# Optimization experiments

Hardware: AMD Instinct MI355X
Metric: run time of the kernel (lower is better)

The kernel has to match this reference:

```python
import jax, jax.numpy as jnp
import numpy as np

SIGMA = 25.0
EPS = 1e-5
TWO_PI = 2.0 * np.pi


def _gn(x, gamma, beta, groups):
    # GroupNorm over (C//G, H, W) per group, per-channel affine.
    B, C, H, W = x.shape
    xg = x.reshape(B, groups, -1)
    m = xg.mean(-1, keepdims=True)
    v = xg.var(-1, keepdims=True)
    xn = ((xg - m) * jax.lax.rsqrt(v + EPS)).reshape(B, C, H, W)
    return xn * gamma[None, :, None, None] + beta[None, :, None, None]


def _conv3(x, k, b):
    y = jax.lax.conv_general_dilated(x, k, (1, 1), 'SAME',
                                     dimension_numbers=('NCHW', 'OIHW', 'NCHW'))
    return y + b[None, :, None, None]


def _tconv2(x, k, b):
    # ConvTranspose2d kernel=2 stride=2 (no overlap) == einsum + reshape.
    # k: [C_in, C_out, 2, 2]
    B, C, H, W = x.shape
    O = k.shape[1]
    y = jnp.einsum('bchw,codq->bohdwq', x, k).reshape(B, O, 2 * H, 2 * W)
    return y + b[None, :, None, None]


def _conv1(x, k, b):
    # 1x1 conv; k: [C_out, C_in]
    return jnp.einsum('bchw,oc->bohw', x, k) + b[None, :, None, None]


def _pool(x):
    B, C, H, W = x.shape
    return x.reshape(B, C, H // 2, 2, W // 2, 2).max(axis=(3, 5))


def _std(t):
    return jnp.sqrt((SIGMA ** (2.0 * t) - 1.0) / (2.0 * jnp.log(SIGMA)))


def setup_inputs() -> dict:
    key = jax.random.key(0)
    ks = jax.random.split(key, 16)
    B, H, W = 64, 128, 128
    E = 2 * W  # 256 = embed_dim

    def w(k, shape, fan_in):
        return jax.random.normal(k, shape, jnp.float32) / np.sqrt(fan_in)

    inp = {
        'x': jax.random.normal(ks[0], (B, 1, H, W), jnp.float32),
        't': jax.random.uniform(ks[1], (B,), jnp.float32, 1e-3, 1.0),
        'Wf': jax.random.normal(ks[2], (H, W), jnp.float32) * 30.0,  # fixed Fourier features
        'fc1_w': w(ks[3], (E, E), E),
        'fc1_b': jnp.zeros((E,), jnp.float32),
        'conv1_k': w(ks[4], (6, 1, 3, 3), 9),
        'conv1_b': jnp.zeros((6,), jnp.float32),
        'gn1_g': jnp.ones((6,), jnp.float32), 'gn1_b': jnp.zeros((6,), jnp.float32),
        'conv2_k': w(ks[5], (24, 6, 3, 3), 6 * 9),
        'conv2_b': jnp.zeros((24,), jnp.float32),
        'gn2_g': jnp.ones((24,), jnp.float32), 'gn2_b': jnp.zeros((24,), jnp.float32),
        't3_k': w(ks[6], (24, 24, 2, 2), 24 * 4),
        't3_b': jnp.zeros((24,), jnp.float32),
        'gn3_g': jnp.ones((48,), jnp.float32), 'gn3_b': jnp.zeros((48,), jnp.float32),
        't4_k': w(ks[7], (48, 12, 2, 2), 48 * 4),
        't4_b': jnp.zeros((12,), jnp.float32),
        'gn4_g': jnp.ones((18,), jnp.float32), 'gn4_b': jnp.zeros((18,), jnp.float32),
        't5_k': w(ks[8], (6, 18), 18),
        't5_b': jnp.zeros((6,), jnp.float32),
        'gn5_g': jnp.ones((6,), jnp.float32), 'gn5_b': jnp.zeros((6,), jnp.float32),
        'fin_k': w(ks[9], (1, 6), 6),
        'fin_b': jnp.zeros((1,), jnp.float32),
    }
    return inp


def reference(x, t, Wf, fc1_w, fc1_b, conv1_k, conv1_b, gn1_g, gn1_b,
              conv2_k, conv2_b, gn2_g, gn2_b, t3_k, t3_b, gn3_g, gn3_b,
              t4_k, t4_b, gn4_g, gn4_b, t5_k, t5_b, gn5_g, gn5_b,
              fin_k, fin_b):
    # Vectorized Gaussian Fourier projection: [B,1,H,W] -> [B,1,H,2W]
    p = x * Wf[None, None] * TWO_PI
    xe = jnp.concatenate([jnp.sin(p), jnp.cos(p)], axis=-1)
    # fc1 on last dim (embed_dim = 2W)
    xf = jnp.einsum('bchw,ow->bcho', xe, fc1_w) + fc1_b
    c1 = _conv3(xf, conv1_k, conv1_b)                              # [B,6,H,2W]
    p1 = _pool(jax.nn.relu(_gn(c1, gn1_g, gn1_b, 6)))              # [B,6,H/2,W]
    c2 = _conv3(p1, conv2_k, conv2_b)                              # [B,24,H/2,W]
    p2 = _pool(jax.nn.relu(_gn(c2, gn2_g, gn2_b, 24)))             # [B,24,H/4,W/2]
    a = p2 * jax.nn.sigmoid(p2)                                    # SiLU bottleneck
    u3 = _tconv2(a, t3_k, t3_b)                                    # [B,24,H/2,W]
    g3 = _gn(jnp.concatenate([c2, u3], axis=1), gn3_g, gn3_b, 6)   # 48 ch
    u4 = _tconv2(g3, t4_k, t4_b)                                   # [B,12,H,2W]
    g4 = _gn(jnp.concatenate([c1, u4], axis=1), gn4_g, gn4_b, 6)   # 18 ch
    u5 = _conv1(g4, t5_k, t5_b)                                    # [B,6,H,2W]
    g5 = _gn(u5, gn5_g, gn5_b, 6)
    return _conv1(g5, fin_k, fin_b) / _std(t)[:, None, None, None]
```

## Files before the change

kernel.cpp:

```cpp
#include <hip/hip_runtime.h>
#include <hip/hip_bf16.h>
#include <math.h>

#define BB 64
#define HH 128
#define WW 128
#define EE 256
#define HP (HH*EE)
#define H2 64
#define W2 128
#define PL2 (H2*W2)
#define H4 32
#define W4 64
#define PL4 (H4*W4)

typedef __hip_bfloat16 bf;
typedef unsigned short ushortt;
typedef __attribute__((ext_vector_type(8))) __bf16 b8v;
typedef __attribute__((ext_vector_type(4))) float f4v;

__device__ __forceinline__ float tof(bf v)    { return __bfloat162float(v); }
__device__ __forceinline__ bf    tob(float v) { return __float2bfloat16(v); }
__device__ __forceinline__ unsigned int bfbits(float v) {
    return (unsigned int)__builtin_bit_cast(ushortt, __float2bfloat16(v));
}
__device__ __forceinline__ float b2f(unsigned int u16) {
    unsigned int x = u16 << 16;
    return __builtin_bit_cast(float, x);
}
__device__ __forceinline__ void wred2(float& s, float& q) {
    #pragma unroll
    for (int m = 32; m; m >>= 1) {
        s += __shfl_xor(s, m);
        q += __shfl_xor(q, m);
    }
}

__global__ __launch_bounds__(256) void k_fourier_fc1(
    const float* __restrict__ x, const float* __restrict__ Wf,
    const float* __restrict__ fc1_w, const float* __restrict__ fc1_b,
    bf* __restrict__ xf, float* __restrict__ mb)
{
    __shared__ ushortt sA[64*264];
    __shared__ ushortt sB[64*264];
    int t = threadIdx.x;
    for (int i = blockIdx.x*256 + t; i < 9216; i += 512*256) mb[i] = 0.f;
    int rb = blockIdx.x >> 2, cb = blockIdx.x & 3;
    int row0 = rb*64, col0 = cb*64;
    const float TP = 6.2831853071795864769f;
    for (int it = 0; it < 32; ++it) {
        int i = it*256 + t;
        int r = i >> 7, w = i & 127;
        int rg = row0 + r;
        float p = x[(size_t)rg*WW + w] * Wf[(size_t)(rg & (HH-1))*WW + w] * TP;
        sA[r*264 + w]       = (ushortt)bfbits(__sinf(p));
        sA[r*264 + 128 + w] = (ushortt)bfbits(__cosf(p));
    }
    #pragma unroll
    for (int it = 0; it < 16; ++it) {
        int i = it*256 + t;
        int o = i >> 6, c4 = i & 63;
        float4 w4 = *(const float4*)(fc1_w + (size_t)(col0 + o)*EE + c4*4);
        uint2 pk;
        pk.x = bfbits(w4.x) | (bfbits(w4.y) << 16);
        pk.y = bfbits(w4.z) | (bfbits(w4.w) << 16);
        *(uint2*)&sB[o*264 + c4*4] = pk;
    }
    __syncthreads();
    int lane = t & 63, wid = t >> 6;
    int m = lane & 15, kq = (lane >> 4) * 8;
    f4v acc[4] = {};
    const ushortt* aBase = &sA[(wid*16 + m)*264 + kq];
    #pragma unroll
    for (int k0 = 0; k0 < 8; ++k0) {
        b8v av = *(const b8v*)(aBase + k0*32);
        #pragma unroll
        for (int t4 = 0; t4 < 4; ++t4) {
            b8v bv = *(const b8v*)&sB[(t4*16 + m)*264 + k0*32 + kq];
            acc[t4] = __builtin_amdgcn_mfma_f32_16x16x32_bf16(av, bv, acc[t4], 0, 0, 0);
        }
    }
    int rbase = row0 + wid*16 + (lane >> 4)*4;
    #pragma unroll
    for (int t4 = 0; t4 < 4; ++t4) {
        int col = col0 + t4*16 + m;
        float bias = fc1_b[col];
        #pragma unroll
        for (int r = 0; r < 4; ++r)
            xf[(size_t)(rbase + r)*EE + col] = tob(acc[t4][r] + bias);
    }
}

__global__ __launch_bounds__(256) void k_conv1(
    const bf* __restrict__ xf, const float* __restrict__ k,
    const float* __restrict__ bias, bf* __restrict__ c1, float* __restrict__ mc1)
{
    __shared__ ushortt sT[6*272];
    __shared__ float red[4][6][2];
    int t = threadIdx.x;
    int ht = blockIdx.x & 31, b = blockIdx.x >> 5;
    int h0 = ht*4;
    const bf* src = xf + (size_t)b*HP;
    if (t < 192) {
        int r = t >> 5, i = t & 31;
        int gy = h0 - 1 + r;
        uint4 v = {0,0,0,0};
        if (gy >= 0 && gy < HH) v = *(const uint4*)(src + (size_t)gy*EE + i*8);
        *(uint4*)&sT[r*272 + 8 + i*8] = v;
    } else if (t < 204) {
        int e = t - 192;
        int r = e >> 1, s = e & 1;
        uint4 z = {0,0,0,0};
        *(uint4*)&sT[r*272 + s*264] = z;
    }
    __syncthreads();
    int wq = (t & 63)*4, hl = t >> 6;
    int lane = t & 63, wid = t >> 6;
    float v[3][6];
    #pragma unroll
    for (int ky = 0; ky < 3; ++ky)
      #pragma unroll
      for (int j = 0; j < 6; ++j)
        v[ky][j] = b2f((unsigned)sT[(hl+ky)*272 + 7 + wq + j]);
    int h = h0 + hl;
    #pragma unroll
    for (int o = 0; o < 6; ++o) {
        float bv = bias[o];
        float a0=bv, a1=bv, a2=bv, a3=bv;
        #pragma unroll
        for (int ky = 0; ky < 3; ++ky)
          #pragma unroll
          for (int kx = 0; kx < 3; ++kx) {
            float wv = k[o*9 + ky*3 + kx];
            a0 += v[ky][kx+0]*wv;
            a1 += v[ky][kx+1]*wv;
            a2 += v[ky][kx+2]*wv;
            a3 += v[ky][kx+3]*wv;
          }
        uint2 pk;
        pk.x = bfbits(a0) | (bfbits(a1) << 16);
        pk.y = bfbits(a2) | (bfbits(a3) << 16);
        *(uint2*)(c1 + ((size_t)(b*6+o)*HH + h)*EE + wq) = pk;
        float s = a0+a1+a2+a3, q = a0*a0+a1*a1+a2*a2+a3*a3;
        wred2(s, q);
        if (lane == 0) { red[wid][o][0] = s; red[wid][o][1] = q; }
    }
    __syncthreads();
    if (t < 6) {
        float S = 0.f, Q = 0.f;
        #pragma unroll
        for (int wv = 0; wv < 4; ++wv) { S += red[wv][t][0]; Q += red[wv][t][1]; }
        atomicAdd(&mc1[((size_t)b*6 + t)*2],     S);
        atomicAdd(&mc1[((size_t)b*6 + t)*2 + 1], Q);
    }
}

__global__ __launch_bounds__(256) void k_conv2(
    const bf* __restrict__ c1, const float* __restrict__ mc1,
    const float* __restrict__ g1, const float* __restrict__ be1,
    const float* __restrict__ kw, const float* __restrict__ bias,
    bf* __restrict__ c2, float* __restrict__ mc2)
{
    __shared__ ushortt sA[256*64];
    __shared__ ushortt sW[32*64];
    __shared__ ushortt sP[6*4*136];
    __shared__ float ssl[12];
    __shared__ float redS[24], redQ[24];
    int t = threadIdx.x;
    int ht = blockIdx.x & 31, b = blockIdx.x >> 5;
    int h0 = ht*2;
    int lane = t & 63, wid = t >> 6;
    int m = lane & 15, q4 = lane >> 4;
    if (t < 24) { redS[t] = 0.f; redQ[t] = 0.f; }
    if (t < 6) {
        float s = mc1[((size_t)b*6 + t)*2], q = mc1[((size_t)b*6 + t)*2 + 1];
        float mean = s * (1.f/HP);
        float var  = q * (1.f/HP) - mean*mean;
        float rstd = rsqrtf(var + 1e-5f);
        float sc = g1[t]*rstd;
        ssl[t*2] = sc; ssl[t*2+1] = be1[t] - mean*sc;
    }
    for (int i = t; i < 1024; i += 256) ((unsigned*)sW)[i] = 0;
    __syncthreads();
    for (int i = t; i < 3120; i += 256) {
        int c = i / 520, rem = i % 520;
        int ry = rem / 130, rx = rem % 130;
        int gy = h0 - 1 + ry, gx = rx - 1;
        float v = 0.f;
        if (gy >= 0 && gy < H2 && gx >= 0 && gx < W2) {
            const bf* pp = c1 + ((size_t)(b*6+c)*HH + 2*gy)*EE + 2*gx;
            unsigned r0 = *(const unsigned*)pp;
            unsigned r1 = *(const unsigned*)(pp + EE);
            float sc = ssl[c*2], sh = ssl[c*2+1];
            float e0 = fmaxf(b2f(r0 & 0xffff)*sc+sh, 0.f);
            float e1 = fmaxf(b2f(r0 >> 16)   *sc+sh, 0.f);
            float e2 = fmaxf(b2f(r1 & 0xffff)*sc+sh, 0.f);
            float e3 = fmaxf(b2f(r1 >> 16)   *sc+sh, 0.f);
            v = fmaxf(fmaxf(e0,e1), fmaxf(e2,e3));
        }
        sP[c*544 + ry*136 + rx] = (ushortt)bfbits(v);
    }
    for (int e = t; e < 1296; e += 256) {
        int o = e / 54, kk = e % 54;
        sW[o*64 + ((((kk >> 3) ^ (o & 7)) << 3) | (kk & 7))] = (ushortt)bfbits(kw[e]);
    }
    __syncthreads();
    {
        int r = t >> 7, xx = t & 127;
        unsigned u[32];
        #pragma unroll
        for (int p = 0; p < 27; ++p) {
            int k0 = 2*p, k1 = 2*p + 1;
            int c0 = k0/9, y0 = (k0%9)/3, x0 = k0%3;
            int c1i = k1/9, y1 = (k1%9)/3, x1 = k1%3;
            unsigned lo = sP[c0*544 + (r+y0)*136 + xx + x0];
            unsigned hi = sP[c1i*544 + (r+y1)*136 + xx + x1];
            u[p] = lo | (hi << 16);
        }
        #pragma unroll
        for (int p = 27; p < 32; ++p) u[p] = 0;
        #pragma unroll
        for (int e = 0; e < 8; ++e) {
            uint4 pk; pk.x = u[4*e]; pk.y = u[4*e+1]; pk.z = u[4*e+2]; pk.w = u[4*e+3];
            *(uint4*)&sA[t*64 + ((e ^ (t & 7)) << 3)] = pk;
        }
    }
    __syncthreads();
    b8v wv[2][2];
    #pragma unroll
    for (int nt = 0; nt < 2; ++nt) {
        int o = nt*16 + m;
        #pragma unroll
        for (int ks = 0; ks < 2; ++ks)
            wv[nt][ks] = *(const b8v*)&sW[o*64 + (((ks*4 + q4) ^ (o & 7)) << 3)];
    }
    f4v acc[4][2] = {};
    #pragma unroll
    for (int mt = 0; mt < 4; ++mt) {
        int px = wid*64 + mt*16 + m;
        b8v a0 = *(const b8v*)&sA[px*64 + (((q4)     ^ (px & 7)) << 3)];
        b8v a1 = *(const b8v*)&sA[px*64 + (((4 + q4) ^ (px & 7)) << 3)];
        #pragma unroll
        for (int nt = 0; nt < 2; ++nt) {
            acc[mt][nt] = __builtin_amdgcn_mfma_f32_16x16x32_bf16(a0, wv[nt][0], acc[mt][nt], 0, 0, 0);
            acc[mt][nt] = __builtin_amdgcn_mfma_f32_16x16x32_bf16(a1, wv[nt][1], acc[mt][nt], 0, 0, 0);
        }
    }
    float sAcc[2] = {0.f, 0.f}, qAcc[2] = {0.f, 0.f};
    #pragma unroll
    for (int nt = 0; nt < 2; ++nt) {
        int o = nt*16 + m;
        bool valid = (o < 24);
        float bo = valid ? bias[o] : 0.f;
        #pragma unroll
        for (int mt = 0; mt < 4; ++mt) {
            int pxb = wid*64 + mt*16 + q4*4;
            unsigned l0 = bfbits(acc[mt][nt][0] + bo);
            unsigned l1 = bfbits(acc[mt][nt][1] + bo);
            unsigned l2 = bfbits(acc[mt][nt][2] + bo);
            unsigned l3 = bfbits(acc[mt][nt][3] + bo);
            if (valid) {
                uint2 pk; pk.x = l0 | (l1 << 16); pk.y = l2 | (l3 << 16);
                int r = pxb >> 7, xx = pxb & 127;
                *(uint2*)(c2 + ((size_t)(b*24+o))*PL2 + (size_t)(h0 + r)*W2 + xx) = pk;
                float f0 = b2f(l0), f1 = b2f(l1), f2 = b2f(l2), f3 = b2f(l3);
                sAcc[nt] += f0+f1+f2+f3;
                qAcc[nt] += f0*f0+f1*f1+f2*f2+f3*f3;
            }
        }
    }
    #pragma unroll
    for (int nt = 0; nt < 2; ++nt) {
        int o = nt*16 + m;
        float s = sAcc[nt], q = qAcc[nt];
        s += __shfl_xor(s, 16); q += __shfl_xor(q, 16);
        s += __shfl_xor(s, 32); q += __shfl_xor(q, 32);
        if (q4 == 0 && o < 24) { atomicAdd(&redS[o], s); atomicAdd(&redQ[o], q); }
    }
    __syncthreads();
    if (t < 24) {
        atomicAdd(&mc2[((size_t)b*24 + t)*2],     redS[t]);
        atomicAdd(&mc2[((size_t)b*24 + t)*2 + 1], redQ[t]);
    }
}

__global__ __launch_bounds__(256) void k_tconv3(
    const bf* __restrict__ c2, const float* __restrict__ mc2,
    const float* __restrict__ g2, const float* __restrict__ be2,
    const float* __restrict__ k3, const float* __restrict__ b3,
    bf* __restrict__ u3, float* __restrict__ mu3)
{
    __shared__ ushortt sA[256*64];
    __shared__ ushortt sW[96*64];
    __shared__ float redS[24], redQ[24];
    __shared__ float ssl[48];
    int t = threadIdx.x;
    int b = blockIdx.x >> 3, pg = blockIdx.x & 7;
    int lane = t & 63, wid = t >> 6;
    int m = lane & 15, q4 = lane >> 4;
    if (t < 24) {
        redS[t] = 0.f; redQ[t] = 0.f;
        float s = mc2[((size_t)b*24 + t)*2], q = mc2[((size_t)b*24 + t)*2 + 1];
        float mean = s * (1.f/PL2);
        float var  = q * (1.f/PL2) - mean*mean;
        float rstd = rsqrtf(var + 1e-5f);
        float sc = g2[t]*rstd;
        ssl[t*2] = sc; ssl[t*2+1] = be2[t] - mean*sc;
    }
    if (t < 96) {
        uint4 z = {0,0,0,0};
        *(uint4*)&sW[t*64 + (((3 ^ (t & 3)) + (t & 4)) << 3)] = z;
    }
    #pragma unroll
    for (int j = 0; j < 9; ++j) {
        int e = j*256 + t;
        int c = e / 96, n = e % 96;
        sW[n*64 + (((((c >> 3) ^ (n & 3)) + (n & 4)) << 3) | (c & 7))] =
            (ushortt)bfbits(k3[e]);
    }
    {
        int pix = pg*256 + t;
        int h4 = pix >> 6, w4 = pix & 63;
        const bf* base = c2 + (size_t)b*24*PL2 + (size_t)(2*h4)*W2 + 2*w4;
        #pragma unroll
        for (int g = 0; g < 3; ++g) {
            unsigned pr[4];
            #pragma unroll
            for (int hc = 0; hc < 4; ++hc) {
                unsigned two[2];
                #pragma unroll
                for (int cc = 0; cc < 2; ++cc) {
                    int c = g*8 + hc*2 + cc;
                    const bf* pp = base + (size_t)c*PL2;
                    unsigned r0 = *(const unsigned*)pp;
                    unsigned r1 = *(const unsigned*)(pp + W2);
                    float sc = ssl[c*2], sh = ssl[c*2+1];
                    float e0 = fmaxf(b2f(r0 & 0xffff)*sc+sh, 0.f);
                    float e1 = fmaxf(b2f(r0 >> 16)   *sc+sh, 0.f);
                    float e2 = fmaxf(b2f(r1 & 0xffff)*sc+sh, 0.f);
                    float e3 = fmaxf(b2f(r1 >> 16)   *sc+sh, 0.f);
                    float mm = fmaxf(fmaxf(e0,e1), fmaxf(e2,e3));
                    mm = mm / (1.f + expf(-mm));
                    two[cc] = bfbits(mm);
                }
                pr[hc] = two[0] | (two[1] << 16);
            }
            uint4 pk; pk.x = pr[0]; pk.y = pr[1]; pk.z = pr[2]; pk.w = pr[3];
            *(uint4*)&sA[t*64 + (((g ^ (t & 3)) + (t & 4)) << 3)] = pk;
        }
        uint4 z = {0,0,0,0};
        *(uint4*)&sA[t*64 + (((3 ^ (t & 3)) + (t & 4)) << 3)] = z;
    }
    __syncthreads();
    b8v wv[6];
    #pragma unroll
    for (int nt = 0; nt < 6; ++nt) {
        int n = nt*16 + m;
        wv[nt] = *(const b8v*)&sW[n*64 + (((q4 ^ (n & 3)) + (n & 4)) << 3)];
    }
    f4v acc[4][6] = {};
    #pragma unroll
    for (int mt = 0; mt < 4; ++mt) {
        int px = wid*64 + mt*16 + m;
        b8v av = *(const b8v*)&sA[px*64 + (((q4 ^ (px & 3)) + (px & 4)) << 3)];
        #pragma unroll
        for (int nt = 0; nt < 6; ++nt)
            acc[mt][nt] = __builtin_amdgcn_mfma_f32_16x16x32_bf16(av, wv[nt], acc[mt][nt], 0, 0, 0);
    }
    float sAcc[6] = {}, qAcc[6] = {};
    int qq = m & 1;
    #pragma unroll
    for (int nt = 0; nt < 6; ++nt) {
        int n = nt*16 + m;
        int o = n >> 2, d = (n >> 1) & 1;
        float bo = b3[o];
        #pragma unroll
        for (int mt = 0; mt < 4; ++mt) {
            int pxb = wid*64 + mt*16 + q4*4;
            unsigned wds[4];
            float s = 0.f, q = 0.f;
            #pragma unroll
            for (int r = 0; r < 4; ++r) {
                float v = acc[mt][nt][r] + bo;
                float vp = __shfl_xor(v, 1);
                unsigned lo = bfbits(v), hi = bfbits(vp);
                wds[r] = lo | (hi << 16);
                float f0 = b2f(lo), f1 = b2f(hi);
                s += f0 + f1;
                q += f0*f0 + f1*f1;
            }
            if (qq == 0) {
                int h4 = (pg*256 + pxb) >> 6;
                int w4 = pxb & 63;
                uint4 pk; pk.x = wds[0]; pk.y = wds[1]; pk.z = wds[2]; pk.w = wds[3];
                *(uint4*)(u3 + ((size_t)(b*24 + o))*PL2 + (size_t)(2*h4 + d)*W2 + 2*w4) = pk;
                sAcc[nt] += s; qAcc[nt] += q;
            }
        }
    }
    #pragma unroll
    for (int nt = 0; nt < 6; ++nt) {
        float s = sAcc[nt], q = qAcc[nt];
        s += __shfl_xor(s, 2);  q += __shfl_xor(q, 2);
        s += __shfl_xor(s, 16); q += __shfl_xor(q, 16);
        s += __shfl_xor(s, 32); q += __shfl_xor(q, 32);
        if ((lane & 51) == 0) {
            int o = nt*4 + (m >> 2);
            atomicAdd(&redS[o], s);
            atomicAdd(&redQ[o], q);
        }
    }
    __syncthreads();
    if (t < 24) {
        atomicAdd(&mu3[((size_t)b*24 + t)*2],     redS[t]);
        atomicAdd(&mu3[((size_t)b*24 + t)*2 + 1], redQ[t]);
    }
}

__global__ __launch_bounds__(256) void k_tconv4(
    const bf* __restrict__ c2, const bf* __restrict__ u3,
    const float* __restrict__ mc2, const float* __restrict__ mu3,
    const float* __restrict__ g3, const float* __restrict__ be3,
    const float* __restrict__ k4, const float* __restrict__ bias4,
    bf* __restrict__ u4, float* __restrict__ mu4)
{
    __shared__ ushortt sA[256*64];
    __shared__ ushortt sW[48*64];
    __shared__ float redS[12], redQ[12];
    __shared__ float ssl[96];
    int t = threadIdx.x;
    int b = blockIdx.x >> 5, pg = blockIdx.x & 31;
    int lane = t & 63, wid = t >> 6;
    int m = lane & 15, q4 = lane >> 4;
    if (t < 12) { redS[t] = 0.f; redQ[t] = 0.f; }
    if (t < 6) {
        float s = 0.f, q = 0.f;
        #pragma unroll
        for (int cl = 0; cl < 8; ++cl) {
            int gc = t*8 + cl;
            const float* p = (gc < 24) ? mc2 + ((size_t)b*24 + gc)*2
                                       : mu3 + ((size_t)b*24 + gc - 24)*2;
            s += p[0]; q += p[1];
        }
        float inv_n = 1.f/((float)PL2*8.f);
        float mean = s*inv_n;
        float var  = q*inv_n - mean*mean;
        float rstd = rsqrtf(var + 1e-5f);
        #pragma unroll
        for (int cl = 0; cl < 8; ++cl) {
            int gc = t*8 + cl;
            float sc = g3[gc]*rstd;
            ssl[gc*2] = sc; ssl[gc*2+1] = be3[gc] - mean*sc;
        }
    }
    #pragma unroll
    for (int j = 0; j < 9; ++j) {
        int e = j*256 + t;
        int c = e / 48, n = e % 48;
        sW[n*64 + ((((c >> 3) ^ (n & 7)) << 3) | (c & 7))] = (ushortt)bfbits(k4[e]);
    }
    if (t < 96) {
        uint4 z = {0,0,0,0};
        int n = t >> 1, kb = 6 + (t & 1);
        *(uint4*)&sW[n*64 + ((kb ^ (n & 7)) << 3)] = z;
    }
    {
        int px = t;
        int pix = pg*256 + px;
        const bf* c2p = c2 + (size_t)b*24*PL2 + pix;
        const bf* u3p = u3 + (size_t)b*24*PL2 + pix;
        #pragma unroll
        for (int g = 0; g < 6; ++g) {
            unsigned pr[4];
            #pragma unroll
            for (int hc = 0; hc < 4; ++hc) {
                int c0 = g*8 + hc*2;
                float r0 = (c0 < 24) ? tof(c2p[(size_t)c0*PL2]) : tof(u3p[(size_t)(c0-24)*PL2]);
                float r1 = (c0+1 < 24) ? tof(c2p[(size_t)(c0+1)*PL2]) : tof(u3p[(size_t)(c0+1-24)*PL2]);
                float v0 = r0 * ssl[2*c0]   + ssl[2*c0+1];
                float v1 = r1 * ssl[2*c0+2] + ssl[2*c0+3];
                pr[hc] = bfbits(v0) | (bfbits(v1) << 16);
            }
            uint4 pk; pk.x = pr[0]; pk.y = pr[1]; pk.z = pr[2]; pk.w = pr[3];
            *(uint4*)&sA[px*64 + ((g ^ (px & 7)) << 3)] = pk;
        }
        uint4 z = {0,0,0,0};
        *(uint4*)&sA[px*64 + ((6 ^ (px & 7)) << 3)] = z;
        *(uint4*)&sA[px*64 + ((7 ^ (px & 7)) << 3)] = z;
    }
    __syncthreads();
    b8v bfr[3][2];
    #pragma unroll
    for (int nt = 0; nt < 3; ++nt) {
        int n = nt*16 + m;
        #pragma unroll
        for (int ks = 0; ks < 2; ++ks)
            bfr[nt][ks] = *(const b8v*)&sW[n*64 + (((ks*4 + q4) ^ (n & 7)) << 3)];
    }
    f4v acc[4][3] = {};
    #pragma unroll
    for (int mt = 0; mt < 4; ++mt) {
        int px = wid*64 + mt*16 + m;
        b8v a0 = *(const b8v*)&sA[px*64 + (((q4)     ^ (px & 7)) << 3)];
        b8v a1 = *(const b8v*)&sA[px*64 + (((4 + q4) ^ (px & 7)) << 3)];
        #pragma unroll
        for (int nt = 0; nt < 3; ++nt) {
            acc[mt][nt] = __builtin_amdgcn_mfma_f32_16x16x32_bf16(a0, bfr[nt][0], acc[mt][nt], 0, 0, 0);
            acc[mt][nt] = __builtin_amdgcn_mfma_f32_16x16x32_bf16(a1, bfr[nt][1], acc[mt][nt], 0, 0, 0);
        }
    }
    float sAcc[3] = {0.f, 0.f, 0.f}, qAcc[3] = {0.f, 0.f, 0.f};
    int qq = m & 1;
    #pragma unroll
    for (int nt = 0; nt < 3; ++nt) {
        int n = nt*16 + m;
        int o = n >> 2, d = (n >> 1) & 1;
        float bo = bias4[o];
        #pragma unroll
        for (int mt = 0; mt < 4; ++mt) {
            int pxb = wid*64 + mt*16 + q4*4;
            unsigned wds[4];
            float s = 0.f, q = 0.f;
            #pragma unroll
            for (int r = 0; r < 4; ++r) {
                float v = acc[mt][nt][r] + bo;
                float vp = __shfl_xor(v, 1);
                unsigned lo = bfbits(v), hi = bfbits(vp);
                wds[r] = lo | (hi << 16);
                float f0 = b2f(lo), f1 = b2f(hi);
                s += f0 + f1;
                q += f0*f0 + f1*f1;
            }
            if (qq == 0) {
                int h2 = (pg*256 + pxb) >> 7;
                int w0 = pxb & 127;
                uint4 pk; pk.x = wds[0]; pk.y = wds[1]; pk.z = wds[2]; pk.w = wds[3];
                *(uint4*)(u4 + (((size_t)(b*12 + o))*HH + 2*h2 + d)*EE + 2*w0) = pk;
                sAcc[nt] += s; qAcc[nt] += q;
            }
        }
    }
    #pragma unroll
    for (int nt = 0; nt < 3; ++nt) {
        float s = sAcc[nt], q = qAcc[nt];
        s += __shfl_xor(s, 2);  q += __shfl_xor(q, 2);
        s += __shfl_xor(s, 16); q += __shfl_xor(q, 16);
        s += __shfl_xor(s, 32); q += __shfl_xor(q, 32);
        if ((lane & 51) == 0) {
            int o = nt*4 + (m >> 2);
            atomicAdd(&redS[o], s);
            atomicAdd(&redQ[o], q);
        }
    }
    __syncthreads();
    if (t < 12) {
        atomicAdd(&mu4[((size_t)b*12 + t)*2],     redS[t]);
        atomicAdd(&mu4[((size_t)b*12 + t)*2 + 1], redQ[t]);
    }
}

__global__ __launch_bounds__(256) void k_conv1x1_u5(
    const bf* __restrict__ c1, const bf* __restrict__ u4,
    const float* __restrict__ mc1, const float* __restrict__ mu4,
    const float* __restrict__ g4, const float* __restrict__ be4,
    const float* __restrict__ k, const float* __restrict__ bias,
    bf* __restrict__ u5, float* __restrict__ mu5)
{
    __shared__ float red[4][6][2];
    __shared__ float ssl[36];
    int t = threadIdx.x;
    int b  = blockIdx.x >> 4;
    int pg = blockIdx.x & 15;
    int pix = pg*2048 + t*8;
    int lane = t & 63, wid = t >> 6;
    if (t < 6) {
        float s = 0.f, q = 0.f;
        #pragma unroll
        for (int cl = 0; cl < 3; ++cl) {
            int gc = t*3 + cl;
            const float* p = (gc < 6) ? mc1 + ((size_t)b*6 + gc)*2
                                      : mu4 + ((size_t)b*12 + gc - 6)*2;
            s += p[0]; q += p[1];
        }
        float inv_n = 1.f/((float)HP*3.f);
        float mean = s*inv_n;
        float var  = q*inv_n - mean*mean;
        float rstd = rsqrtf(var + 1e-5f);
        #pragma unroll
        for (int cl = 0; cl < 3; ++cl) {
            int gc = t*3 + cl;
            float sc = g4[gc]*rstd;
            ssl[gc*2] = sc; ssl[gc*2+1] = be4[gc] - mean*sc;
        }
    }
    __syncthreads();
    const bf* c1p = c1 + ((size_t)b*6)*HP + pix;
    const bf* u4p = u4 + ((size_t)b*12)*HP + pix;
    float acc[6][8];
    #pragma unroll
    for (int o = 0; o < 6; ++o) {
        float bv = bias[o];
        #pragma unroll
        for (int j = 0; j < 8; ++j) acc[o][j] = bv;
    }
    #pragma unroll
    for (int c = 0; c < 18; ++c) {
        uint4 r = (c < 6) ? *(const uint4*)(c1p + (size_t)c*HP)
                          : *(const uint4*)(u4p + (size_t)(c-6)*HP);
        float sc = ssl[2*c], sh = ssl[2*c+1];
        float v[8];
        v[0] = b2f(r.x & 0xffff)*sc + sh;  v[1] = b2f(r.x >> 16)*sc + sh;
        v[2] = b2f(r.y & 0xffff)*sc + sh;  v[3] = b2f(r.y >> 16)*sc + sh;
        v[4] = b2f(r.z & 0xffff)*sc + sh;  v[5] = b2f(r.z >> 16)*sc + sh;
        v[6] = b2f(r.w & 0xffff)*sc + sh;  v[7] = b2f(r.w >> 16)*sc + sh;
        #pragma unroll
        for (int o = 0; o < 6; ++o) {
            float wv = k[o*18 + c];
            #pragma unroll
            for (int j = 0; j < 8; ++j) acc[o][j] += v[j]*wv;
        }
    }
    #pragma unroll
    for (int o = 0; o < 6; ++o) {
        uint4 pk;
        pk.x = bfbits(acc[o][0]) | (bfbits(acc[o][1]) << 16);
        pk.y = bfbits(acc[o][2]) | (bfbits(acc[o][3]) << 16);
        pk.z = bfbits(acc[o][4]) | (bfbits(acc[o][5]) << 16);
        pk.w = bfbits(acc[o][6]) | (bfbits(acc[o][7]) << 16);
        *(uint4*)(u5 + ((size_t)(b*6+o))*HP + pix) = pk;
        float s = 0.f, q = 0.f;
        #pragma unroll
        for (int j = 0; j < 8; ++j) { s += acc[o][j]; q += acc[o][j]*acc[o][j]; }
        wred2(s, q);
        if (lane == 0) { red[wid][o][0] = s; red[wid][o][1] = q; }
    }
    __syncthreads();
    if (t < 6) {
        float S = 0.f, Q = 0.f;
        #pragma unroll
        for (int wv = 0; wv < 4; ++wv) { S += red[wv][t][0]; Q += red[wv][t][1]; }
        atomicAdd(&mu5[((size_t)b*6 + t)*2],     S);
        atomicAdd(&mu5[((size_t)b*6 + t)*2 + 1], Q);
    }
}

__global__ __launch_bounds__(256) void k_final(
    const bf* __restrict__ u5, const float* __restrict__ mu5,
    const float* __restrict__ g5, const float* __restrict__ be5,
    const float* __restrict__ k, const float* __restrict__ bias,
    const float* __restrict__ t, float* __restrict__ out)
{
    __shared__ float ssl[12];
    int tt = threadIdx.x;
    int b = blockIdx.x >> 4;
    int pix = ((blockIdx.x & 15)*256 + tt)*8;
    if (tt < 6) {
        float s = mu5[((size_t)b*6 + tt)*2], q = mu5[((size_t)b*6 + tt)*2 + 1];
        float mean = s * (1.f/HP);
        float var  = q * (1.f/HP) - mean*mean;
        float rstd = rsqrtf(var + 1e-5f);
        float sc = g5[tt]*rstd;
        ssl[tt*2] = sc; ssl[tt*2+1] = be5[tt] - mean*sc;
    }
    __syncthreads();
    const bf* up = u5 + (size_t)b*6*HP + pix;
    float bv = bias[0];
    float a[8];
    #pragma unroll
    for (int j = 0; j < 8; ++j) a[j] = bv;
    #pragma unroll
    for (int c = 0; c < 6; ++c) {
        uint4 r = *(const uint4*)(up + (size_t)c*HP);
        float sc = ssl[2*c], sh = ssl[2*c+1];
        float wv = k[c];
        a[0] += (b2f(r.x & 0xffff)*sc + sh) * wv;
        a[1] += (b2f(r.x >> 16)   *sc + sh) * wv;
        a[2] += (b2f(r.y & 0xffff)*sc + sh) * wv;
        a[3] += (b2f(r.y >> 16)   *sc + sh) * wv;
        a[4] += (b2f(r.z & 0xffff)*sc + sh) * wv;
        a[5] += (b2f(r.z >> 16)   *sc + sh) * wv;
        a[6] += (b2f(r.w & 0xffff)*sc + sh) * wv;
        a[7] += (b2f(r.w >> 16)   *sc + sh) * wv;
    }
    float tb = t[b];
    const float lns = 3.2188758248682007492f;
    float var = (expf(2.f*tb*lns) - 1.f) / (2.f*lns);
    float rs = rsqrtf(var);
    float4 o0; o0.x = a[0]*rs; o0.y = a[1]*rs; o0.z = a[2]*rs; o0.w = a[3]*rs;
    float4 o1; o1.x = a[4]*rs; o1.y = a[5]*rs; o1.z = a[6]*rs; o1.w = a[7]*rs;
    float* op = out + (size_t)b*HP + pix;
    *(float4*)op       = o0;
    *(float4*)(op + 4) = o1;
}

extern "C" void kernel_launch(void* const* d_in, const int* in_sizes, int n_in,
                              void* d_out, int out_size, void* d_ws, size_t ws_size,
                              hipStream_t stream)
{
    const float* x       = (const float*)d_in[0];
    const float* t       = (const float*)d_in[1];
    const float* Wf      = (const float*)d_in[2];
    const float* fc1_w   = (const float*)d_in[3];
    const float* fc1_b   = (const float*)d_in[4];
    const float* conv1_k = (const float*)d_in[5];
    const float* conv1_b = (const float*)d_in[6];
    const float* gn1_g   = (const float*)d_in[7];
    const float* gn1_b   = (const float*)d_in[8];
    const float* conv2_k = (const float*)d_in[9];
    const float* conv2_b = (const float*)d_in[10];
    const float* gn2_g   = (const float*)d_in[11];
    const float* gn2_b   = (const float*)d_in[12];
    const float* t3_k    = (const float*)d_in[13];
    const float* t3_b    = (const float*)d_in[14];
    const float* gn3_g   = (const float*)d_in[15];
    const float* gn3_b   = (const float*)d_in[16];
    const float* t4_k    = (const float*)d_in[17];
    const float* t4_b    = (const float*)d_in[18];
    const float* gn4_g   = (const float*)d_in[19];
    const float* gn4_b   = (const float*)d_in[20];
    const float* t5_k    = (const float*)d_in[21];
    const float* t5_b    = (const float*)d_in[22];
    const float* gn5_g   = (const float*)d_in[23];
    const float* gn5_b   = (const float*)d_in[24];
    const float* fin_k   = (const float*)d_in[25];
    const float* fin_b   = (const float*)d_in[26];

    bf* wsb = (bf*)d_ws;
    bf* c1 = wsb;
    bf* c2 = wsb + 12582912;
    bf* u3 = wsb + 25165824;
    bf* u4 = wsb + 37748736;
    bf* xf = wsb + 39845888;
    bf* u5 = wsb + 12582912;
    float* mb = (float*)(wsb + 62914560);
    float* mc1 = mb;
    float* mc2 = mb + 768;
    float* mu3 = mb + 3840;
    float* mu4 = mb + 6912;
    float* mu5 = mb + 8448;

    k_fourier_fc1<<<512, 256, 0, stream>>>(x, Wf, fc1_w, fc1_b, xf, mb);
    k_conv1<<<2048, 256, 0, stream>>>(xf, conv1_k, conv1_b, c1, mc1);
    k_conv2<<<2048, 256, 0, stream>>>(c1, mc1, gn1_g, gn1_b,
                                      conv2_k, conv2_b, c2, mc2);
    k_tconv3<<<512, 256, 0, stream>>>(c2, mc2, gn2_g, gn2_b,
                                      t3_k, t3_b, u3, mu3);
    k_tconv4<<<2048, 256, 0, stream>>>(c2, u3, mc2, mu3, gn3_g, gn3_b,
                                       t4_k, t4_b, u4, mu4);
    k_conv1x1_u5<<<1024, 256, 0, stream>>>(c1, u4, mc1, mu4, gn4_g, gn4_b,
                                           t5_k, t5_b, u5, mu5);
    k_final<<<1024, 256, 0, stream>>>(u5, mu5, gn5_g, gn5_b,
                                      fin_k, fin_b, t, (float*)d_out);
}
```

Measured before the change: 234.0 us.

## Fuse 1x1 conv u5 and final head with per-batch grid barrier

Merges the u5 1x1 conv and the final GN+1x1+scale kernel into a single kernel. Each block handles twice as many pixels and keeps u5 in registers. The per-batch GroupNorm statistics are completed through an atomic counter spin-wait among the 8 blocks of each batch, which removes the bf16 u5 write and re-read and one launch. The spin-wait relies on all 8 blocks of a batch being co-resident and could deadlock if they are not scheduled together. It also adds a counter that is zeroed in the first kernel.

```diff
diff --git a/kernel.cpp b/kernel.cpp
--- a/kernel.cpp
+++ b/kernel.cpp
@@ -44,7 +44,7 @@
     __shared__ ushortt sA[64*264];
     __shared__ ushortt sB[64*264];
     int t = threadIdx.x;
-    for (int i = blockIdx.x*256 + t; i < 9216; i += 512*256) mb[i] = 0.f;
+    for (int i = blockIdx.x*256 + t; i < 9280; i += 512*256) mb[i] = 0.f;
     int rb = blockIdx.x >> 2, cb = blockIdx.x & 3;
     int row0 = rb*64, col0 = cb*64;
     const float TP = 6.2831853071795864769f;
@@ -559,19 +559,23 @@
     }
 }
 
-__global__ __launch_bounds__(256) void k_conv1x1_u5(
+__global__ __launch_bounds__(256, 2) void k_head(
     const bf* __restrict__ c1, const bf* __restrict__ u4,
     const float* __restrict__ mc1, const float* __restrict__ mu4,
     const float* __restrict__ g4, const float* __restrict__ be4,
     const float* __restrict__ k, const float* __restrict__ bias,
-    bf* __restrict__ u5, float* __restrict__ mu5)
+    const float* __restrict__ g5, const float* __restrict__ be5,
+    const float* __restrict__ kf, const float* __restrict__ fbv,
+    const float* __restrict__ tv,
+    float* __restrict__ mu5, unsigned* __restrict__ cnt,
+    float* __restrict__ out)
 {
     __shared__ float red[4][6][2];
     __shared__ float ssl[36];
+    __shared__ float ssl5[12];
     int t = threadIdx.x;
-    int b  = blockIdx.x >> 4;
-    int pg = blockIdx.x & 15;
-    int pix = pg*2048 + t*8;
+    int b   = blockIdx.x >> 3;
+    int sub = blockIdx.x & 7;
     int lane = t & 63, wid = t >> 6;
     if (t < 6) {
         float s = 0.f, q = 0.f;
@@ -594,43 +598,47 @@
         }
     }
     __syncthreads();
-    const bf* c1p = c1 + ((size_t)b*6)*HP + pix;
-    const bf* u4p = u4 + ((size_t)b*12)*HP + pix;
-    float acc[6][8];
+    int pixA = sub*4096 + t*8;
+    float acc[2][6][8];
+    #pragma unroll
+    for (int ch = 0; ch < 2; ++ch) {
+        int pix = pixA + ch*2048;
+        const bf* c1p = c1 + ((size_t)b*6)*HP + pix;
+        const bf* u4p = u4 + ((size_t)b*12)*HP + pix;
+        #pragma unroll
+        for (int o = 0; o < 6; ++o) {
+            float bv = bias[o];
+            #pragma unroll
+            for (int j = 0; j < 8; ++j) acc[ch][o][j] = bv;
+        }
+        #pragma unroll
+        for (int c = 0; c < 18; ++c) {
+            uint4 r = (c < 6) ? *(const uint4*)(c1p + (size_t)c*HP)
+                              : *(const uint4*)(u4p + (size_t)(c-6)*HP);
+            float sc = ssl[2*c], sh = ssl[2*c+1];
+            float v[8];
+            v[0] = b2f(r.x & 0xffff)*sc + sh;  v[1] = b2f(r.x >> 16)*sc + sh;
+            v[2] = b2f(r.y & 0xffff)*sc + sh;  v[3] = b2f(r.y >> 16)*sc + sh;
+            v[4] = b2f(r.z & 0xffff)*sc + sh;  v[5] = b2f(r.z >> 16)*sc + sh;
+            v[6] = b2f(r.w & 0xffff)*sc + sh;  v[7] = b2f(r.w >> 16)*sc + sh;
+            #pragma unroll
+            for (int o = 0; o < 6; ++o) {
+                float wv = k[o*18 + c];
+                #pragma unroll
+                for (int j = 0; j < 8; ++j) acc[ch][o][j] += v[j]*wv;
+            }
+        }
+    }
     #pragma unroll
     for (int o = 0; o < 6; ++o) {
-        float bv = bias[o];
-        #pragma unroll
-        for (int j = 0; j < 8; ++j) acc[o][j] = bv;
-    }
-    #pragma unroll
-    for (int c = 0; c < 18; ++c) {
-        uint4 r = (c < 6) ? *(const uint4*)(c1p + (size_t)c*HP)
-                          : *(const uint4*)(u4p + (size_t)(c-6)*HP);
-        float sc = ssl[2*c], sh = ssl[2*c+1];
-        float v[8];
-        v[0] = b2f(r.x & 0xffff)*sc + sh;  v[1] = b2f(r.x >> 16)*sc + sh;
-        v[2] = b2f(r.y & 0xffff)*sc + sh;  v[3] = b2f(r.y >> 16)*sc + sh;
-        v[4] = b2f(r.z & 0xffff)*sc + sh;  v[5] = b2f(r.z >> 16)*sc + sh;
-        v[6] = b2f(r.w & 0xffff)*sc + sh;  v[7] = b2f(r.w >> 16)*sc + sh;
-        #pragma unroll
-        for (int o = 0; o < 6; ++o) {
-            float wv = k[o*18 + c];
-            #pragma unroll
-            for (int j = 0; j < 8; ++j) acc[o][j] += v[j]*wv;
-        }
-    }
-    #pragma unroll
-    for (int o = 0; o < 6; ++o) {
-        uint4 pk;
-        pk.x = bfbits(acc[o][0]) | (bfbits(acc[o][1]) << 16);
-        pk.y = bfbits(acc[o][2]) | (bfbits(acc[o][3]) << 16);
-        pk.z = bfbits(acc[o][4]) | (bfbits(acc[o][5]) << 16);
-        pk.w = bfbits(acc[o][6]) | (bfbits(acc[o][7]) << 16);
-        *(uint4*)(u5 + ((size_t)(b*6+o))*HP + pix) = pk;
         float s = 0.f, q = 0.f;
         #pragma unroll
-        for (int j = 0; j < 8; ++j) { s += acc[o][j]; q += acc[o][j]*acc[o][j]; }
+        for (int ch = 0; ch < 2; ++ch)
+          #pragma unroll
+          for (int j = 0; j < 8; ++j) {
+            float a = acc[ch][o][j];
+            s += a; q += a*a;
+          }
         wred2(s, q);
         if (lane == 0) { red[wid][o][0] = s; red[wid][o][1] = q; }
     }
@@ -642,55 +650,50 @@
         atomicAdd(&mu5[((size_t)b*6 + t)*2],     S);
         atomicAdd(&mu5[((size_t)b*6 + t)*2 + 1], Q);
     }
-}
-
-__global__ __launch_bounds__(256) void k_final(
-    const bf* __restrict__ u5, const float* __restrict__ mu5,
-    const float* __restrict__ g5, const float* __restrict__ be5,
-    const float* __restrict__ k, const float* __restrict__ bias,
-    const float* __restrict__ t, float* __restrict__ out)
-{
-    __shared__ float ssl[12];
-    int tt = threadIdx.x;
-    int b = blockIdx.x >> 4;
-    int pix = ((blockIdx.x & 15)*256 + tt)*8;
-    if (tt < 6) {
-        float s = mu5[((size_t)b*6 + tt)*2], q = mu5[((size_t)b*6 + tt)*2 + 1];
+    __syncthreads();
+    if (t == 0) {
+        __threadfence();
+        atomicAdd(&cnt[b], 1u);
+        while (__hip_atomic_load(&cnt[b], __ATOMIC_ACQUIRE,
+                                 __HIP_MEMORY_SCOPE_AGENT) < 8u)
+            __builtin_amdgcn_s_sleep(16);
+    }
+    __syncthreads();
+    if (t < 6) {
+        float s = __hip_atomic_load(&mu5[((size_t)b*6 + t)*2],
+                                    __ATOMIC_RELAXED, __HIP_MEMORY_SCOPE_AGENT);
+        float q = __hip_atomic_load(&mu5[((size_t)b*6 + t)*2 + 1],
+                                    __ATOMIC_RELAXED, __HIP_MEMORY_SCOPE_AGENT);
         float mean = s * (1.f/HP);
         float var  = q * (1.f/HP) - mean*mean;
         float rstd = rsqrtf(var + 1e-5f);
-        float sc = g5[tt]*rstd;
-        ssl[tt*2] = sc; ssl[tt*2+1] = be5[tt] - mean*sc;
-    }
-    __syncthreads();
-    const bf* up = u5 + (size_t)b*6*HP + pix;
-    float bv = bias[0];
-    float a[8];
-    #pragma unroll
-    for (int j = 0; j < 8; ++j) a[j] = bv;
-    #pragma unroll
-    for (int c = 0; c < 6; ++c) {
-        uint4 r = *(const uint4*)(up + (size_t)c*HP);
-        float sc = ssl[2*c], sh = ssl[2*c+1];
-        float wv = k[c];
-        a[0] += (b2f(r.x & 0xffff)*sc + sh) * wv;
-        a[1] += (b2f(r.x >> 16)   *sc + sh) * wv;
-        a[2] += (b2f(r.y & 0xffff)*sc + sh) * wv;
-        a[3] += (b2f(r.y >> 16)   *sc + sh) * wv;
-        a[4] += (b2f(r.z & 0xffff)*sc + sh) * wv;
-        a[5] += (b2f(r.z >> 16)   *sc + sh) * wv;
-        a[6] += (b2f(r.w & 0xffff)*sc + sh) * wv;
-        a[7] += (b2f(r.w >> 16)   *sc + sh) * wv;
-    }
-    float tb = t[b];
+        float sc = g5[t]*rstd;
+        ssl5[t*2] = sc; ssl5[t*2+1] = be5[t] - mean*sc;
+    }
+    __syncthreads();
+    float tb = tv[b];
     const float lns = 3.2188758248682007492f;
-    float var = (expf(2.f*tb*lns) - 1.f) / (2.f*lns);
-    float rs = rsqrtf(var);
-    float4 o0; o0.x = a[0]*rs; o0.y = a[1]*rs; o0.z = a[2]*rs; o0.w = a[3]*rs;
-    float4 o1; o1.x = a[4]*rs; o1.y = a[5]*rs; o1.z = a[6]*rs; o1.w = a[7]*rs;
-    float* op = out + (size_t)b*HP + pix;
-    *(float4*)op       = o0;
-    *(float4*)(op + 4) = o1;
+    float varr = (expf(2.f*tb*lns) - 1.f) / (2.f*lns);
+    float rs = rsqrtf(varr);
+    float base = fbv[0];
+    #pragma unroll
+    for (int ch = 0; ch < 2; ++ch) {
+        int pix = pixA + ch*2048;
+        float ov[8];
+        #pragma unroll
+        for (int j = 0; j < 8; ++j) {
+            float v = base;
+            #pragma unroll
+            for (int o = 0; o < 6; ++o)
+                v += kf[o] * (acc[ch][o][j]*ssl5[2*o] + ssl5[2*o+1]);
+            ov[j] = v*rs;
+        }
+        float* op = out + (size_t)b*HP + pix;
+        float4 o0; o0.x = ov[0]; o0.y = ov[1]; o0.z = ov[2]; o0.w = ov[3];
+        float4 o1; o1.x = ov[4]; o1.y = ov[5]; o1.z = ov[6]; o1.w = ov[7];
+        *(float4*)op       = o0;
+        *(float4*)(op + 4) = o1;
+    }
 }
 
 extern "C" void kernel_launch(void* const* d_in, const int* in_sizes, int n_in,
@@ -731,13 +734,13 @@
     bf* u3 = wsb + 25165824;
     bf* u4 = wsb + 37748736;
     bf* xf = wsb + 39845888;
-    bf* u5 = wsb + 12582912;
     float* mb = (float*)(wsb + 62914560);
     float* mc1 = mb;
     float* mc2 = mb + 768;
     float* mu3 = mb + 3840;
     float* mu4 = mb + 6912;
     float* mu5 = mb + 8448;
+    unsigned* cnt = (unsigned*)(mb + 9216);
 
     k_fourier_fc1<<<512, 256, 0, stream>>>(x, Wf, fc1_w, fc1_b, xf, mb);
     k_conv1<<<2048, 256, 0, stream>>>(xf, conv1_k, conv1_b, c1, mc1);
@@ -747,8 +750,7 @@
                                       t3_k, t3_b, u3, mu3);
     k_tconv4<<<2048, 256, 0, stream>>>(c2, u3, mc2, mu3, gn3_g, gn3_b,
                                        t4_k, t4_b, u4, mu4);
-    k_conv1x1_u5<<<1024, 256, 0, stream>>>(c1, u4, mc1, mu4, gn4_g, gn4_b,
-                                           t5_k, t5_b, u5, mu5);
-    k_final<<<1024, 256, 0, stream>>>(u5, mu5, gn5_g, gn5_b,
-                                      fin_k, fin_b, t, (float*)d_out);
-}
+    k_head<<<512, 256, 0, stream>>>(c1, u4, mc1, mu4, gn4_g, gn4_b,
+                                    t5_k, t5_b, gn5_g, gn5_b,
+                                    fin_k, fin_b, t, mu5, cnt, (float*)d_out);
+}
```

Result: slower. 421.9 us (+80.2%).
